# Performance work log

Hardware: AMD Instinct MI355X
Metric: run time of the kernel (lower is better)

## Reference

```python
import jax, jax.numpy as jnp
import numpy as np
import math

D_MODEL = 512
DIM_K = 512
DIM_V = 512
N_HEADS = 8


def setup_inputs() -> dict:
    key = jax.random.key(0)
    ks = jax.random.split(key, 12)
    B, S = 2, 2048
    sc = 1.0 / math.sqrt(D_MODEL)
    return {
        "x": jax.random.normal(ks[0], (B, S, D_MODEL), dtype=jnp.float32),
        "y": jax.random.normal(ks[1], (B, S, D_MODEL), dtype=jnp.float32),
        # weights stored [in, out] so linear is x @ W + b
        "Wq": jax.random.normal(ks[2], (D_MODEL, DIM_K), dtype=jnp.float32) * sc,
        "bq": jnp.zeros((DIM_K,), dtype=jnp.float32),
        "Wk": jax.random.normal(ks[3], (D_MODEL, DIM_K), dtype=jnp.float32) * sc,
        "bk": jnp.zeros((DIM_K,), dtype=jnp.float32),
        "Wv": jax.random.normal(ks[4], (D_MODEL, DIM_V), dtype=jnp.float32) * sc,
        "bv": jnp.zeros((DIM_V,), dtype=jnp.float32),
        "Wo": jax.random.normal(ks[5], (DIM_V, D_MODEL), dtype=jnp.float32) * sc,
        "bo": jnp.zeros((D_MODEL,), dtype=jnp.float32),
    }


def reference(x, y, Wq, bq, Wk, bk, Wv, bv, Wo, bo):
    B, S, _ = x.shape
    H = N_HEADS
    Dh = DIM_K // H
    Dvh = DIM_V // H
    norm = 1.0 / math.sqrt(D_MODEL)  # note: original scales by 1/sqrt(d_model)

    # torch: q(x).reshape(-1, B, S, Dh) -> heads on leading dim (row-major)
    Q = (x @ Wq + bq).reshape(-1, B, S, Dh)      # [H,B,S,Dh]
    K = (y @ Wk + bk).reshape(-1, B, S, Dh)      # [H,B,S,Dh]
    V = (y @ Wv + bv).reshape(-1, B, S, Dvh)     # [H,B,S,Dvh]

    scores = jnp.einsum('hbqd,hbkd->hbqk', Q, K) * norm  # [H,B,S,S]

    # median-threshold mask: torch.median on even n returns lower middle value
    med_idx = (S - 1) // 2
    thre = jnp.sort(scores, axis=-1)[..., med_idx:med_idx + 1]  # [H,B,S,1]
    masked = scores - thre <= 0  # mask where score <= median
    scores = jnp.where(masked, -jnp.inf, scores)

    attn = jax.nn.softmax(scores, axis=-1)
    # dropout omitted (deterministic / eval mode)
    out = jnp.einsum('hbqk,hbkd->hbqd', attn, V)  # [H,B,S,Dvh]
    out = out.reshape(B, S, -1)                   # faithful row-major reshape
    return out @ Wo + bo
```

## Files before the change

kernel.cpp:

```cpp
#include <hip/hip_runtime.h>
#include <hip/hip_bf16.h>
#include <stdint.h>

#define SEQ    2048
#define DMODEL 512
#define NPANEL 16
#define NORM   0.044194173824159216f

typedef _Float16 f16;
typedef __attribute__((ext_vector_type(8))) _Float16 half8;
typedef __attribute__((ext_vector_type(2))) _Float16 half2v;
typedef __attribute__((ext_vector_type(4))) float f32x4;
typedef __attribute__((ext_vector_type(4))) unsigned int u32x4;

__device__ __forceinline__ unsigned umin2(unsigned a, unsigned b){ return a<b?a:b; }
__device__ __forceinline__ unsigned umax2(unsigned a, unsigned b){ return a>b?a:b; }

__global__ __launch_bounds__(256) void k_cvt(const float4* __restrict__ x,
                                             const float4* __restrict__ y,
                                             f16* __restrict__ xh, f16* __restrict__ xl,
                                             f16* __restrict__ yh, f16* __restrict__ yl){
  int i = blockIdx.x*256 + threadIdx.x;
  float4 a = x[i]; float4 b = y[i];
  half2v h0 = {(f16)a.x, (f16)a.y}, h1 = {(f16)a.z, (f16)a.w};
  *(half2v*)(xh + i*4)     = h0; *(half2v*)(xh + i*4 + 2) = h1;
  half2v l0 = {(f16)(a.x-(float)h0[0]), (f16)(a.y-(float)h0[1])};
  half2v l1 = {(f16)(a.z-(float)h1[0]), (f16)(a.w-(float)h1[1])};
  *(half2v*)(xl + i*4)     = l0; *(half2v*)(xl + i*4 + 2) = l1;
  half2v g0 = {(f16)b.x, (f16)b.y}, g1 = {(f16)b.z, (f16)b.w};
  *(half2v*)(yh + i*4)     = g0; *(half2v*)(yh + i*4 + 2) = g1;
  half2v m0 = {(f16)(b.x-(float)g0[0]), (f16)(b.y-(float)g0[1])};
  half2v m1 = {(f16)(b.z-(float)g1[0]), (f16)(b.w-(float)g1[1])};
  *(half2v*)(yl + i*4)     = m0; *(half2v*)(yl + i*4 + 2) = m1;
}

__global__ __launch_bounds__(256) void k_wt(const float* __restrict__ Wq, const float* __restrict__ Wk,
                                            const float* __restrict__ Wv, const float* __restrict__ Wo,
                                            f16* __restrict__ Wth, f16* __restrict__ Wtl){
  int z = blockIdx.z;
  const float* W = (z==0)?Wq:(z==1)?Wk:(z==2)?Wv:Wo;
  __shared__ float tile[64][65];
  int k0 = blockIdx.x*64, n0 = blockIdx.y*64;
  #pragma unroll
  for (int i = 0; i < 16; ++i){
    int s = threadIdx.x + i*256; int kl2 = s>>6, nl = s&63;
    tile[kl2][nl] = W[(k0+kl2)*512 + (n0+nl)];
  }
  __syncthreads();
  #pragma unroll
  for (int i = 0; i < 16; ++i){
    int s = threadIdx.x + i*256; int nl = s>>6, kl2 = s&63;
    float v = tile[kl2][nl];
    f16 h = (f16)v;
    int idx = z*262144 + (n0+nl)*512 + (k0+kl2);
    Wth[idx] = h;
    Wtl[idx] = (f16)(v - (float)h);
  }
}

template<int FINAL>
__global__ __launch_bounds__(256) void k_gemm(const f16* __restrict__ Ah0, const f16* __restrict__ Al0,
                                              const f16* __restrict__ Ah1, const f16* __restrict__ Al1,
                                              const f16* __restrict__ Wh, const f16* __restrict__ Wl,
                                              const float* __restrict__ b0, const float* __restrict__ b1,
                                              const float* __restrict__ b2,
                                              f16* __restrict__ Oq, float* __restrict__ Of){
  int z = blockIdx.z;
  const f16* A  = (z==0) ? Ah0 : Ah1;
  const f16* Alp= (z==0) ? Al0 : Al1;
  const f16* Bh = Wh + z*262144;
  const f16* Bl = Wl + z*262144;
  const float* bias = (z==0)?b0:(z==1)?b1:b2;
  const bool split = (FINAL==0) && (z<2);
  int m0 = blockIdx.x*128, n0 = blockIdx.y*128;

  __shared__ f16 Ahs[128][40], Bhs[128][40], Als[128][40], Bls[128][40];

  int t = threadIdx.x, l = t&63, w = t>>6;
  int wr = w>>1, wc = w&1;
  int lr = l&15, lk = l>>4;

  f32x4 acc[4][4];
  #pragma unroll
  for (int i=0;i<4;++i)
    #pragma unroll
    for (int j=0;j<4;++j) acc[i][j] = (f32x4){0.f,0.f,0.f,0.f};

  for (int ks = 0; ks < 16; ++ks){
    int k0 = ks*32;
    #pragma unroll
    for (int i = 0; i < 2; ++i){
      int s = t + i*256; int r = s>>2, kc = s&3;
      *(u32x4*)(&Ahs[r][kc*8]) = *(const u32x4*)(A   + (m0+r)*512 + k0 + kc*8);
      *(u32x4*)(&Bhs[r][kc*8]) = *(const u32x4*)(Bh  + (n0+r)*512 + k0 + kc*8);
      if (split){
        *(u32x4*)(&Als[r][kc*8]) = *(const u32x4*)(Alp + (m0+r)*512 + k0 + kc*8);
        *(u32x4*)(&Bls[r][kc*8]) = *(const u32x4*)(Bl  + (n0+r)*512 + k0 + kc*8);
      }
    }
    __syncthreads();
    half8 ah[4], bh2[4], al2[4], bl2[4];
    #pragma unroll
    for (int tm = 0; tm < 4; ++tm) ah[tm]  = *(const half8*)(&Ahs[wr*64 + tm*16 + lr][lk*8]);
    #pragma unroll
    for (int tn = 0; tn < 4; ++tn) bh2[tn] = *(const half8*)(&Bhs[wc*64 + tn*16 + lr][lk*8]);
    if (split){
      #pragma unroll
      for (int tm = 0; tm < 4; ++tm) al2[tm] = *(const half8*)(&Als[wr*64 + tm*16 + lr][lk*8]);
      #pragma unroll
      for (int tn = 0; tn < 4; ++tn) bl2[tn] = *(const half8*)(&Bls[wc*64 + tn*16 + lr][lk*8]);
    }
    #pragma unroll
    for (int tm = 0; tm < 4; ++tm)
      #pragma unroll
      for (int tn = 0; tn < 4; ++tn){
        acc[tm][tn] = __builtin_amdgcn_mfma_f32_16x16x32_f16(ah[tm], bh2[tn], acc[tm][tn], 0,0,0);
        if (split){
          acc[tm][tn] = __builtin_amdgcn_mfma_f32_16x16x32_f16(ah[tm], bl2[tn], acc[tm][tn], 0,0,0);
          acc[tm][tn] = __builtin_amdgcn_mfma_f32_16x16x32_f16(al2[tm], bh2[tn], acc[tm][tn], 0,0,0);
        }
      }
    __syncthreads();
  }

  #pragma unroll
  for (int tn = 0; tn < 4; ++tn){
    int n_g = n0 + wc*64 + tn*16 + lr;
    float bv = bias[n_g];
    #pragma unroll
    for (int tm = 0; tm < 4; ++tm){
      #pragma unroll
      for (int r = 0; r < 4; ++r){
        int m_g = m0 + wr*64 + tm*16 + lk*4 + r;
        float v = acc[tm][tn][r] + bv;
        size_t idx = (size_t)m_g*512 + n_g;
        if (FINAL){
          Of[idx] = v;
        } else if (z < 2){
          f16 h = (f16)v;
          Oq[(size_t)z*4194304 + idx] = h;
          Oq[(size_t)z*4194304 + 2097152 + idx] = (f16)(v - (float)h);
        } else {
          Oq[(size_t)4*2097152 + idx] = (f16)v;
        }
      }
    }
  }
}

__global__ __launch_bounds__(256) void k_vt(const unsigned short* __restrict__ V, unsigned short* __restrict__ Vt){
  int p = blockIdx.y;
  int t = threadIdx.x;
  int d = t & 63, sc = t >> 6;
  int s0b = blockIdx.x*32 + sc*8;
  const unsigned short* Vp = V + p*131072;
  unsigned short* Vtp = Vt + p*131072;
  typedef __attribute__((ext_vector_type(8))) short short8;
  short8 vv;
  #pragma unroll
  for (int j = 0; j < 8; ++j) vv[j] = (short)Vp[(s0b + j)*64 + d];
  *(short8*)(Vtp + d*2048 + s0b) = vv;
}

__global__ __launch_bounds__(512, 4) void k_attn(const f16* __restrict__ Qh, const f16* __restrict__ Ql,
                                                 const f16* __restrict__ Kh, const f16* __restrict__ Kl,
                                                 const f16* __restrict__ Vt, f16* __restrict__ O){
  extern __shared__ char scb[];
  __shared__ float rzs[16];
  __shared__ float red[1024];
  int p = blockIdx.y, qt = blockIdx.x;
  int s0 = qt*16;
  const f16* Qhp = Qh + p*131072;
  const f16* Qlp = Ql + p*131072;
  const f16* Khp = Kh + p*131072;
  const f16* Klp = Kl + p*131072;
  const f16* Vtp = Vt + p*131072;
  int t = threadIdx.x, l = t&63, w = t>>6;
  int lr = l&15, lk = l>>4;

  half8 qh[2], ql[2];
  #pragma unroll
  for (int f = 0; f < 2; ++f){
    qh[f] = *(const half8*)(Qhp + (s0+lr)*64 + f*32 + lk*8);
    ql[f] = *(const half8*)(Qlp + (s0+lr)*64 + f*32 + lk*8);
  }

  {
    int cbase = w*128;
    #pragma unroll 2
    for (int ct = 0; ct < 8; ++ct){
      int n = cbase + ct*16;
      const f16* kb  = Khp + (n+lr)*64 + lk*8;
      const f16* kb2 = Klp + (n+lr)*64 + lk*8;
      half8 kh0 = *(const half8*)(kb),  kh1 = *(const half8*)(kb + 32);
      half8 kl0 = *(const half8*)(kb2), kl1 = *(const half8*)(kb2 + 32);
      f32x4 acc = (f32x4){0.f,0.f,0.f,0.f};
      acc = __builtin_amdgcn_mfma_f32_16x16x32_f16(qh[0], kh0, acc, 0,0,0);
      acc = __builtin_amdgcn_mfma_f32_16x16x32_f16(qh[1], kh1, acc, 0,0,0);
      acc = __builtin_amdgcn_mfma_f32_16x16x32_f16(qh[0], kl0, acc, 0,0,0);
      acc = __builtin_amdgcn_mfma_f32_16x16x32_f16(qh[1], kl1, acc, 0,0,0);
      acc = __builtin_amdgcn_mfma_f32_16x16x32_f16(ql[0], kh0, acc, 0,0,0);
      acc = __builtin_amdgcn_mfma_f32_16x16x32_f16(ql[1], kh1, acc, 0,0,0);
      #pragma unroll
      for (int r = 0; r < 4; ++r){
        int row = lk*4 + r;
        *(float*)(scb + row*4096 + (((unsigned)((n + lr)*4)) ^ ((unsigned)(lk<<6)))) = acc[r];
      }
    }
  }
  __syncthreads();

  unsigned ovA0[16], ovA1[16];
  {
    int row0 = w*2;
    unsigned C = ((unsigned)((row0>>2)&3))<<6;
    const char* rb0 = scb + row0*4096;
    const char* rb1 = rb0 + 4096;
    #pragma unroll
    for (int j = 0; j < 16; ++j){
      unsigned off = (((unsigned)((l + j*64)*4)) ^ C);
      unsigned u0 = *(const unsigned*)(rb0 + off);
      unsigned u1 = *(const unsigned*)(rb1 + off);
      ovA0[j] = ((int)u0 < 0) ? ~u0 : (u0 | 0x80000000u);
      ovA1[j] = ((int)u1 < 0) ? ~u1 : (u1 | 0x80000000u);
    }
  }
  __syncthreads();

  {
    int cbase = w*128;
    #pragma unroll 2
    for (int ct = 0; ct < 8; ++ct){
      int n = cbase + ct*16;
      const f16* kb  = Khp + (1024 + n + lr)*64 + lk*8;
      const f16* kb2 = Klp + (1024 + n + lr)*64 + lk*8;
      half8 kh0 = *(const half8*)(kb),  kh1 = *(const half8*)(kb + 32);
      half8 kl0 = *(const half8*)(kb2), kl1 = *(const half8*)(kb2 + 32);
      f32x4 acc = (f32x4){0.f,0.f,0.f,0.f};
      acc = __builtin_amdgcn_mfma_f32_16x16x32_f16(qh[0], kh0, acc, 0,0,0);
      acc = __builtin_amdgcn_mfma_f32_16x16x32_f16(qh[1], kh1, acc, 0,0,0);
      acc = __builtin_amdgcn_mfma_f32_16x16x32_f16(qh[0], kl0, acc, 0,0,0);
      acc = __builtin_amdgcn_mfma_f32_16x16x32_f16(qh[1], kl1, acc, 0,0,0);
      acc = __builtin_amdgcn_mfma_f32_16x16x32_f16(ql[0], kh0, acc, 0,0,0);
      acc = __builtin_amdgcn_mfma_f32_16x16x32_f16(ql[1], kh1, acc, 0,0,0);
      #pragma unroll
      for (int r = 0; r < 4; ++r){
        int row = lk*4 + r;
        *(float*)(scb + row*4096 + (((unsigned)((n + lr)*4)) ^ ((unsigned)(lk<<6)))) = acc[r];
      }
    }
  }
  __syncthreads();

  #pragma unroll
  for (int rr = 0; rr < 2; ++rr){
    int row = w*2 + rr;
    const char* rb = scb + row*4096;
    unsigned C = ((unsigned)((row>>2)&3))<<6;
    unsigned o2[16];
    #pragma unroll
    for (int j = 0; j < 16; ++j){
      unsigned u = *(const unsigned*)(rb + (((unsigned)((l + j*64)*4)) ^ C));
      o2[j] = ((int)u < 0) ? ~u : (u | 0x80000000u);
    }
    unsigned umn = 0xFFFFFFFFu, umx = 0u;
    #pragma unroll
    for (int j = 0; j < 16; ++j){
      unsigned a = (rr==0) ? ovA0[j] : ovA1[j];
      umn = umin2(umn, umin2(a, o2[j]));
      umx = umax2(umax2(umx, a), o2[j]);
    }
    #pragma unroll
    for (int off2 = 1; off2 < 64; off2 <<= 1){
      umn = umin2(umn, (unsigned)__shfl_xor((int)umn, off2));
      umx = umax2(umax2(umx, (unsigned)__shfl_xor((int)umx, off2)), umx);
    }
    unsigned thr;
    {
      unsigned L = umn, R = umx;
      #pragma unroll 1
      for (;;){
        if (L >= R){ thr = R; break; }
        unsigned mid = L + ((R - L) >> 1);
        int c = 0;
        #pragma unroll
        for (int j = 0; j < 16; ++j){
          unsigned a = (rr==0) ? ovA0[j] : ovA1[j];
          c += (int)__popcll(__ballot(a <= mid));
          c += (int)__popcll(__ballot(o2[j] <= mid));
        }
        if (c == 1024){ thr = mid; break; }
        if (c > 1024) R = mid; else L = mid + 1;
      }
    }
    unsigned bmx = (umx & 0x80000000u) ? (umx & 0x7FFFFFFFu) : ~umx;
    float mx = __uint_as_float(bmx);
    float zs = 0.f;
    unsigned g = ((unsigned)(row & 7)) << 4;
    char* pb = scb + row*4096;
    #pragma unroll
    for (int j = 0; j < 32; ++j){
      unsigned a = (j < 16) ? ((rr==0) ? ovA0[j] : ovA1[j]) : o2[j-16];
      unsigned b = (a & 0x80000000u) ? (a & 0x7FFFFFFFu) : ~a;
      float v = __uint_as_float(b);
      float wgt = (a <= thr) ? 0.f : __expf((v - mx) * NORM);
      zs += wgt;
      unsigned col = (unsigned)((j & 15)*64 + l + (j >> 4)*1024);
      *(f16*)(pb + (((col*2)) ^ g)) = (f16)wgt;
    }
    #pragma unroll
    for (int off2 = 1; off2 < 64; off2 <<= 1) zs += __shfl_xor(zs, off2);
    if (l == 0) rzs[row] = 1.f / zs;
  }
  __syncthreads();

  int oc = w & 3, kh2 = w >> 2;
  f32x4 oa = (f32x4){0.f,0.f,0.f,0.f};
  #pragma unroll 4
  for (int kc = 0; kc < 32; ++kc){
    int kbase = kh2*1024 + kc*32;
    half8 pa = *(const half8*)(scb + lr*4096 + (((unsigned)((kbase + lk*8)*2)) ^ (((unsigned)(lr & 7)) << 4)));
    half8 vb = *(const half8*)(Vtp + (oc*16 + lr)*2048 + kbase + lk*8);
    oa = __builtin_amdgcn_mfma_f32_16x16x32_f16(pa, vb, oa, 0,0,0);
  }
  if (kh2 == 1){
    #pragma unroll
    for (int r = 0; r < 4; ++r) red[oc*256 + (lk*4+r)*16 + lr] = oa[r];
  }
  __syncthreads();
  if (kh2 == 0){
    #pragma unroll
    for (int r = 0; r < 4; ++r){
      int row = lk*4 + r;
      float v = (oa[r] + red[oc*256 + row*16 + lr]) * rzs[row];
      O[p*131072 + (s0+row)*64 + oc*16 + lr] = (f16)v;
    }
  }
}

extern "C" void kernel_launch(void* const* d_in, const int* in_sizes, int n_in,
                              void* d_out, int out_size, void* d_ws, size_t ws_size,
                              hipStream_t stream) {
  const float* x  = (const float*)d_in[0];
  const float* y  = (const float*)d_in[1];
  const float* Wq = (const float*)d_in[2];
  const float* bq = (const float*)d_in[3];
  const float* Wk = (const float*)d_in[4];
  const float* bk = (const float*)d_in[5];
  const float* Wv = (const float*)d_in[6];
  const float* bv = (const float*)d_in[7];
  const float* Wo = (const float*)d_in[8];
  const float* bo = (const float*)d_in[9];

  f16* ws = (f16*)d_ws;
  f16* xh  = ws;
  f16* xl  = ws + 2097152;
  f16* yh  = ws + 4194304;
  f16* yl  = ws + 6291456;
  f16* Wth = ws + 8388608;
  f16* Wtl = ws + 9437184;
  f16* QKV = ws + 10485760;
  f16* Vt  = ws;
  f16* Ob  = ws + 2097152;

  (void)hipFuncSetAttribute(reinterpret_cast<const void*>(k_attn),
                            hipFuncAttributeMaxDynamicSharedMemorySize, 65536);

  k_cvt<<<2048, 256, 0, stream>>>((const float4*)x, (const float4*)y, xh, xl, yh, yl);
  k_wt<<<dim3(8,8,4), 256, 0, stream>>>(Wq, Wk, Wv, Wo, Wth, Wtl);
  k_gemm<0><<<dim3(32,4,3), 256, 0, stream>>>(xh, xl, yh, yl, Wth, Wtl, bq, bk, bv, QKV, nullptr);
  k_vt<<<dim3(64,16), 256, 0, stream>>>((const unsigned short*)(QKV + 4*2097152), (unsigned short*)Vt);
  k_attn<<<dim3(128,16), 512, 65536, stream>>>(QKV, QKV + 2097152, QKV + 2*2097152, QKV + 3*2097152, Vt, Ob);
  k_gemm<1><<<dim3(32,4,1), 256, 0, stream>>>(Ob, Ob, Ob, Ob, Wth + 3*262144, Wtl, bo, bo, bo, nullptr, (float*)d_out);
}
```

Baseline: 289.4 us.

## Split fused attention into score, median-select and PV kernels via workspace

```diff
diff --git a/kernel.cpp b/kernel.cpp
--- a/kernel.cpp
+++ b/kernel.cpp
@@ -162,6 +162,127 @@
   *(short8*)(Vtp + d*2048 + s0b) = vv;
 }
 
+__global__ __launch_bounds__(512, 6) void k_score(const f16* __restrict__ Qh, const f16* __restrict__ Ql,
+                                                  const f16* __restrict__ Kh, const f16* __restrict__ Kl,
+                                                  float* __restrict__ S){
+  int p = blockIdx.x, qt = blockIdx.y;
+  int s0 = qt*16;
+  const f16* Qhp = Qh + p*131072;
+  const f16* Qlp = Ql + p*131072;
+  const f16* Khp = Kh + p*131072;
+  const f16* Klp = Kl + p*131072;
+  int t = threadIdx.x, l = t&63, w = t>>6;
+  int lr = l&15, lk = l>>4;
+
+  half8 qh[2], qlo[2];
+  #pragma unroll
+  for (int f = 0; f < 2; ++f){
+    qh[f]  = *(const half8*)(Qhp + (s0+lr)*64 + f*32 + lk*8);
+    qlo[f] = *(const half8*)(Qlp + (s0+lr)*64 + f*32 + lk*8);
+  }
+  float* Sb = S + (size_t)(p*2048 + s0)*2048;
+
+  #pragma unroll 2
+  for (int ct = 0; ct < 16; ++ct){
+    int n = w*256 + ct*16;
+    const f16* kb = Khp + (n+lr)*64 + lk*8;
+    const f16* lb = Klp + (n+lr)*64 + lk*8;
+    half8 kh0 = *(const half8*)(kb);
+    half8 kh1 = *(const half8*)(kb + 32);
+    half8 kl0 = *(const half8*)(lb);
+    half8 kl1 = *(const half8*)(lb + 32);
+    f32x4 c1 = (f32x4){0.f,0.f,0.f,0.f};
+    f32x4 c2 = (f32x4){0.f,0.f,0.f,0.f};
+    f32x4 c3 = (f32x4){0.f,0.f,0.f,0.f};
+    c1 = __builtin_amdgcn_mfma_f32_16x16x32_f16(qh[0],  kh0, c1, 0,0,0);
+    c2 = __builtin_amdgcn_mfma_f32_16x16x32_f16(qh[0],  kl0, c2, 0,0,0);
+    c3 = __builtin_amdgcn_mfma_f32_16x16x32_f16(qlo[0], kh0, c3, 0,0,0);
+    c1 = __builtin_amdgcn_mfma_f32_16x16x32_f16(qh[1],  kh1, c1, 0,0,0);
+    c2 = __builtin_amdgcn_mfma_f32_16x16x32_f16(qh[1],  kl1, c2, 0,0,0);
+    c3 = __builtin_amdgcn_mfma_f32_16x16x32_f16(qlo[1], kh1, c3, 0,0,0);
+    #pragma unroll
+    for (int r = 0; r < 4; ++r){
+      Sb[(size_t)(lk*4 + r)*2048 + n + lr] = c1[r] + c2[r] + c3[r];
+    }
+  }
+}
+
+__global__ __launch_bounds__(256, 6) void k_sel(const float* S, f16* P, float* __restrict__ rz){
+  int wid = blockIdx.x*4 + (threadIdx.x>>6);
+  int l = threadIdx.x & 63;
+  const float* row = S + (size_t)wid*2048;
+  unsigned ov[32];
+  #pragma unroll
+  for (int j = 0; j < 32; ++j){
+    unsigned u = __float_as_uint(row[l + j*64]);
+    ov[j] = ((int)u < 0) ? ~u : (u | 0x80000000u);
+  }
+  unsigned umn = 0xFFFFFFFFu, umx = 0u;
+  #pragma unroll
+  for (int j = 0; j < 32; ++j){ umn = umin2(umn, ov[j]); umx = umax2(umx, ov[j]); }
+  #pragma unroll
+  for (int off2 = 1; off2 < 64; off2 <<= 1){
+    umn = umin2(umn, (unsigned)__shfl_xor((int)umn, off2));
+    umx = umax2(umx, (unsigned)__shfl_xor((int)umx, off2));
+  }
+  unsigned thr;
+  {
+    unsigned L = umn, R = umx;
+    #pragma unroll 1
+    for (;;){
+      if (L >= R){ thr = R; break; }
+      unsigned mid = L + ((R - L) >> 1);
+      int c = 0;
+      #pragma unroll
+      for (int j = 0; j < 32; ++j) c += (int)__popcll(__ballot(ov[j] <= mid));
+      if (c == 1024){ thr = mid; break; }
+      if (c > 1024) R = mid; else L = mid + 1;
+    }
+  }
+  unsigned bmx = (umx & 0x80000000u) ? (umx & 0x7FFFFFFFu) : ~umx;
+  float mx = __uint_as_float(bmx);
+  float zs = 0.f;
+  f16* prow = P + (size_t)wid*4096;
+  #pragma unroll
+  for (int j = 0; j < 32; ++j){
+    unsigned a = ov[j];
+    unsigned b = (a & 0x80000000u) ? (a & 0x7FFFFFFFu) : ~a;
+    float v = __uint_as_float(b);
+    float wgt = (a <= thr) ? 0.f : __expf((v - mx) * NORM);
+    zs += wgt;
+    prow[l + j*64] = (f16)wgt;
+  }
+  #pragma unroll
+  for (int off2 = 1; off2 < 64; off2 <<= 1) zs += __shfl_xor(zs, off2);
+  if (l == 0) rz[wid] = 1.f / zs;
+}
+
+__global__ __launch_bounds__(512, 8) void k_pv(const f16* __restrict__ P, const f16* __restrict__ Vt,
+                                               const float* __restrict__ rz, f16* __restrict__ O){
+  int p = blockIdx.x, rt = blockIdx.y;
+  int t = threadIdx.x, l = t&63, w = t>>6;
+  int lr = l&15, lk = l>>4;
+  int wr = w>>2, oc = w&3;
+  int r0 = rt*32 + wr*16;
+  const f16* prow = P + (size_t)(p*2048 + r0 + lr)*4096 + lk*8;
+  const f16* vb   = Vt + p*131072 + (oc*16 + lr)*2048 + lk*8;
+  f32x4 o0 = (f32x4){0.f,0.f,0.f,0.f};
+  f32x4 o1 = (f32x4){0.f,0.f,0.f,0.f};
+  #pragma unroll 4
+  for (int kc = 0; kc < 64; ++kc){
+    half8 pa = *(const half8*)(prow + kc*32);
+    half8 vv = *(const half8*)(vb + kc*32);
+    if (kc & 1) o1 = __builtin_amdgcn_mfma_f32_16x16x32_f16(pa, vv, o1, 0,0,0);
+    else        o0 = __builtin_amdgcn_mfma_f32_16x16x32_f16(pa, vv, o0, 0,0,0);
+  }
+  #pragma unroll
+  for (int r = 0; r < 4; ++r){
+    int g = r0 + lk*4 + r;
+    float val = (o0[r] + o1[r]) * rz[p*2048 + g];
+    O[p*131072 + g*64 + oc*16 + lr] = (f16)val;
+  }
+}
+
 __global__ __launch_bounds__(512, 4) void k_attn(const f16* __restrict__ Qh, const f16* __restrict__ Ql,
                                                  const f16* __restrict__ Kh, const f16* __restrict__ Kl,
                                                  const f16* __restrict__ Vt, f16* __restrict__ O){
@@ -252,7 +373,7 @@
   }
   __syncthreads();
 
-  #pragma unroll
+  #pragma unroll 1
   for (int rr = 0; rr < 2; ++rr){
     int row = w*2 + rr;
     const char* rb = scb + row*4096;
@@ -273,7 +394,7 @@
     #pragma unroll
     for (int off2 = 1; off2 < 64; off2 <<= 1){
       umn = umin2(umn, (unsigned)__shfl_xor((int)umn, off2));
-      umx = umax2(umax2(umx, (unsigned)__shfl_xor((int)umx, off2)), umx);
+      umx = umax2(umx, (unsigned)__shfl_xor((int)umx, off2));
     }
     unsigned thr;
     {
@@ -306,7 +427,7 @@
       float wgt = (a <= thr) ? 0.f : __expf((v - mx) * NORM);
       zs += wgt;
       unsigned col = (unsigned)((j & 15)*64 + l + (j >> 4)*1024);
-      *(f16*)(pb + (((col*2)) ^ g)) = (f16)wgt;
+      *(f16*)(pb + ((col*2) ^ g)) = (f16)wgt;
     }
     #pragma unroll
     for (int off2 = 1; off2 < 64; off2 <<= 1) zs += __shfl_xor(zs, off2);
@@ -363,13 +484,28 @@
   f16* Vt  = ws;
   f16* Ob  = ws + 2097152;
 
-  (void)hipFuncSetAttribute(reinterpret_cast<const void*>(k_attn),
-                            hipFuncAttributeMaxDynamicSharedMemorySize, 65536);
+  const size_t S_off  = 41943040ULL;
+  const size_t S_size = 268435456ULL;
+  const size_t rz_off = S_off + S_size;
+  const size_t NEED   = rz_off + 131072ULL;
+  bool use_split = (ws_size >= NEED);
 
   k_cvt<<<2048, 256, 0, stream>>>((const float4*)x, (const float4*)y, xh, xl, yh, yl);
   k_wt<<<dim3(8,8,4), 256, 0, stream>>>(Wq, Wk, Wv, Wo, Wth, Wtl);
   k_gemm<0><<<dim3(32,4,3), 256, 0, stream>>>(xh, xl, yh, yl, Wth, Wtl, bq, bk, bv, QKV, nullptr);
   k_vt<<<dim3(64,16), 256, 0, stream>>>((const unsigned short*)(QKV + 4*2097152), (unsigned short*)Vt);
-  k_attn<<<dim3(128,16), 512, 65536, stream>>>(QKV, QKV + 2097152, QKV + 2*2097152, QKV + 3*2097152, Vt, Ob);
+
+  if (use_split){
+    float* S  = (float*)((char*)d_ws + S_off);
+    float* rz = (float*)((char*)d_ws + rz_off);
+    k_score<<<dim3(16,128), 512, 0, stream>>>(QKV, QKV + 2097152, QKV + 2*2097152, QKV + 3*2097152, S);
+    k_sel<<<dim3(8192), 256, 0, stream>>>(S, (f16*)S, rz);
+    k_pv<<<dim3(16,64), 512, 0, stream>>>((const f16*)S, Vt, rz, Ob);
+  } else {
+    (void)hipFuncSetAttribute(reinterpret_cast<const void*>(k_attn),
+                              hipFuncAttributeMaxDynamicSharedMemorySize, 65536);
+    k_attn<<<dim3(128,16), 512, 65536, stream>>>(QKV, QKV + 2097152, QKV + 2*2097152, QKV + 3*2097152, Vt, Ob);
+  }
+
   k_gemm<1><<<dim3(32,4,1), 256, 0, stream>>>(Ob, Ob, Ob, Ob, Wth + 3*262144, Wtl, bo, bo, bo, nullptr, (float*)d_out);
 }
```

Result: no change. 287.7 us (-0.6%).

## Swap attention grid order and split MFMA accumulators into independent chains

Applied to the files above, without the earlier changes.

```diff
diff --git a/kernel.cpp b/kernel.cpp
--- a/kernel.cpp
+++ b/kernel.cpp
@@ -168,7 +168,7 @@
   extern __shared__ char scb[];
   __shared__ float rzs[16];
   __shared__ float red[1024];
-  int p = blockIdx.y, qt = blockIdx.x;
+  int p = blockIdx.x, qt = blockIdx.y;
   int s0 = qt*16;
   const f16* Qhp = Qh + p*131072;
   const f16* Qlp = Ql + p*131072;
@@ -185,74 +185,53 @@
     ql[f] = *(const half8*)(Qlp + (s0+lr)*64 + f*32 + lk*8);
   }
 
-  {
-    int cbase = w*128;
-    #pragma unroll 2
+  unsigned ovA0[16], ovA1[16];
+
+  #pragma unroll 1
+  for (int ph = 0; ph < 2; ++ph){
+    const f16* ka = Khp + ((ph<<10) + w*128 + lr)*64 + lk*8;
+    const f16* la = Klp + ((ph<<10) + w*128 + lr)*64 + lk*8;
+    int n = w*128 + lr;
+    #pragma unroll 1
     for (int ct = 0; ct < 8; ++ct){
-      int n = cbase + ct*16;
-      const f16* kb  = Khp + (n+lr)*64 + lk*8;
-      const f16* kb2 = Klp + (n+lr)*64 + lk*8;
-      half8 kh0 = *(const half8*)(kb),  kh1 = *(const half8*)(kb + 32);
-      half8 kl0 = *(const half8*)(kb2), kl1 = *(const half8*)(kb2 + 32);
-      f32x4 acc = (f32x4){0.f,0.f,0.f,0.f};
-      acc = __builtin_amdgcn_mfma_f32_16x16x32_f16(qh[0], kh0, acc, 0,0,0);
-      acc = __builtin_amdgcn_mfma_f32_16x16x32_f16(qh[1], kh1, acc, 0,0,0);
-      acc = __builtin_amdgcn_mfma_f32_16x16x32_f16(qh[0], kl0, acc, 0,0,0);
-      acc = __builtin_amdgcn_mfma_f32_16x16x32_f16(qh[1], kl1, acc, 0,0,0);
-      acc = __builtin_amdgcn_mfma_f32_16x16x32_f16(ql[0], kh0, acc, 0,0,0);
-      acc = __builtin_amdgcn_mfma_f32_16x16x32_f16(ql[1], kh1, acc, 0,0,0);
+      half8 kb0 = *(const half8*)(ka);
+      half8 kb1 = *(const half8*)(ka + 32);
+      half8 lb0 = *(const half8*)(la);
+      half8 lb1 = *(const half8*)(la + 32);
+      f32x4 c1 = (f32x4){0.f,0.f,0.f,0.f};
+      f32x4 c2 = (f32x4){0.f,0.f,0.f,0.f};
+      f32x4 c3 = (f32x4){0.f,0.f,0.f,0.f};
+      c1 = __builtin_amdgcn_mfma_f32_16x16x32_f16(qh[0], kb0, c1, 0,0,0);
+      c2 = __builtin_amdgcn_mfma_f32_16x16x32_f16(qh[0], lb0, c2, 0,0,0);
+      c3 = __builtin_amdgcn_mfma_f32_16x16x32_f16(ql[0], kb0, c3, 0,0,0);
+      c1 = __builtin_amdgcn_mfma_f32_16x16x32_f16(qh[1], kb1, c1, 0,0,0);
+      c2 = __builtin_amdgcn_mfma_f32_16x16x32_f16(qh[1], lb1, c2, 0,0,0);
+      c3 = __builtin_amdgcn_mfma_f32_16x16x32_f16(ql[1], kb1, c3, 0,0,0);
       #pragma unroll
       for (int r = 0; r < 4; ++r){
         int row = lk*4 + r;
-        *(float*)(scb + row*4096 + (((unsigned)((n + lr)*4)) ^ ((unsigned)(lk<<6)))) = acc[r];
-      }
-    }
-  }
-  __syncthreads();
-
-  unsigned ovA0[16], ovA1[16];
-  {
-    int row0 = w*2;
-    unsigned C = ((unsigned)((row0>>2)&3))<<6;
-    const char* rb0 = scb + row0*4096;
-    const char* rb1 = rb0 + 4096;
-    #pragma unroll
-    for (int j = 0; j < 16; ++j){
-      unsigned off = (((unsigned)((l + j*64)*4)) ^ C);
-      unsigned u0 = *(const unsigned*)(rb0 + off);
-      unsigned u1 = *(const unsigned*)(rb1 + off);
-      ovA0[j] = ((int)u0 < 0) ? ~u0 : (u0 | 0x80000000u);
-      ovA1[j] = ((int)u1 < 0) ? ~u1 : (u1 | 0x80000000u);
-    }
-  }
-  __syncthreads();
-
-  {
-    int cbase = w*128;
-    #pragma unroll 2
-    for (int ct = 0; ct < 8; ++ct){
-      int n = cbase + ct*16;
-      const f16* kb  = Khp + (1024 + n + lr)*64 + lk*8;
-      const f16* kb2 = Klp + (1024 + n + lr)*64 + lk*8;
-      half8 kh0 = *(const half8*)(kb),  kh1 = *(const half8*)(kb + 32);
-      half8 kl0 = *(const half8*)(kb2), kl1 = *(const half8*)(kb2 + 32);
-      f32x4 acc = (f32x4){0.f,0.f,0.f,0.f};
-      acc = __builtin_amdgcn_mfma_f32_16x16x32_f16(qh[0], kh0, acc, 0,0,0);
-      acc = __builtin_amdgcn_mfma_f32_16x16x32_f16(qh[1], kh1, acc, 0,0,0);
-      acc = __builtin_amdgcn_mfma_f32_16x16x32_f16(qh[0], kl0, acc, 0,0,0);
-      acc = __builtin_amdgcn_mfma_f32_16x16x32_f16(qh[1], kl1, acc, 0,0,0);
-      acc = __builtin_amdgcn_mfma_f32_16x16x32_f16(ql[0], kh0, acc, 0,0,0);
-      acc = __builtin_amdgcn_mfma_f32_16x16x32_f16(ql[1], kh1, acc, 0,0,0);
-      #pragma unroll
-      for (int r = 0; r < 4; ++r){
-        int row = lk*4 + r;
-        *(float*)(scb + row*4096 + (((unsigned)((n + lr)*4)) ^ ((unsigned)(lk<<6)))) = acc[r];
-      }
-    }
-  }
-  __syncthreads();
-
-  #pragma unroll
+        *(float*)(scb + row*4096 + (((unsigned)(n*4)) ^ ((unsigned)(lk<<6)))) = c1[r] + c2[r] + c3[r];
+      }
+      ka += 1024; la += 1024; n += 16;
+    }
+    __syncthreads();
+    if (ph == 0){
+      unsigned C = ((unsigned)((w>>1)&3))<<6;
+      const char* rb0 = scb + (w*2)*4096;
+      const char* rb1 = rb0 + 4096;
+      #pragma unroll
+      for (int j = 0; j < 16; ++j){
+        unsigned off = (((unsigned)((l + j*64)*4)) ^ C);
+        unsigned u0 = *(const unsigned*)(rb0 + off);
+        unsigned u1 = *(const unsigned*)(rb1 + off);
+        ovA0[j] = ((int)u0 < 0) ? ~u0 : (u0 | 0x80000000u);
+        ovA1[j] = ((int)u1 < 0) ? ~u1 : (u1 | 0x80000000u);
+      }
+      __syncthreads();
+    }
+  }
+
+  #pragma unroll 1
   for (int rr = 0; rr < 2; ++rr){
     int row = w*2 + rr;
     const char* rb = scb + row*4096;
@@ -273,7 +252,7 @@
     #pragma unroll
     for (int off2 = 1; off2 < 64; off2 <<= 1){
       umn = umin2(umn, (unsigned)__shfl_xor((int)umn, off2));
-      umx = umax2(umax2(umx, (unsigned)__shfl_xor((int)umx, off2)), umx);
+      umx = umax2(umx, (unsigned)__shfl_xor((int)umx, off2));
     }
     unsigned thr;
     {
@@ -306,7 +285,7 @@
       float wgt = (a <= thr) ? 0.f : __expf((v - mx) * NORM);
       zs += wgt;
       unsigned col = (unsigned)((j & 15)*64 + l + (j >> 4)*1024);
-      *(f16*)(pb + (((col*2)) ^ g)) = (f16)wgt;
+      *(f16*)(pb + ((col*2) ^ g)) = (f16)wgt;
     }
     #pragma unroll
     for (int off2 = 1; off2 < 64; off2 <<= 1) zs += __shfl_xor(zs, off2);
@@ -315,14 +294,25 @@
   __syncthreads();
 
   int oc = w & 3, kh2 = w >> 2;
-  f32x4 oa = (f32x4){0.f,0.f,0.f,0.f};
-  #pragma unroll 4
-  for (int kc = 0; kc < 32; ++kc){
-    int kbase = kh2*1024 + kc*32;
-    half8 pa = *(const half8*)(scb + lr*4096 + (((unsigned)((kbase + lk*8)*2)) ^ (((unsigned)(lr & 7)) << 4)));
-    half8 vb = *(const half8*)(Vtp + (oc*16 + lr)*2048 + kbase + lk*8);
-    oa = __builtin_amdgcn_mfma_f32_16x16x32_f16(pa, vb, oa, 0,0,0);
-  }
+  const f16* vb = Vtp + (oc*16 + lr)*2048 + kh2*1024 + lk*8;
+  const char* pbase = scb + lr*4096;
+  unsigned pswz = ((unsigned)(lr & 7)) << 4;
+  unsigned pk = (unsigned)(kh2*1024 + lk*8);
+  f32x4 o0 = (f32x4){0.f,0.f,0.f,0.f};
+  f32x4 o1 = (f32x4){0.f,0.f,0.f,0.f};
+  #pragma unroll 1
+  for (int it = 0; it < 16; ++it){
+    half8 pa0 = *(const half8*)(pbase + (((pk)*2) ^ pswz));
+    half8 vb0 = *(const half8*)(vb);
+    half8 pa1 = *(const half8*)(pbase + (((pk + 32)*2) ^ pswz));
+    half8 vb1 = *(const half8*)(vb + 32);
+    o0 = __builtin_amdgcn_mfma_f32_16x16x32_f16(pa0, vb0, o0, 0,0,0);
+    o1 = __builtin_amdgcn_mfma_f32_16x16x32_f16(pa1, vb1, o1, 0,0,0);
+    pk += 64; vb += 64;
+  }
+  f32x4 oa;
+  #pragma unroll
+  for (int r = 0; r < 4; ++r) oa[r] = o0[r] + o1[r];
   if (kh2 == 1){
     #pragma unroll
     for (int r = 0; r < 4; ++r) red[oc*256 + (lk*4+r)*16 + lr] = oa[r];
@@ -370,6 +360,6 @@
   k_wt<<<dim3(8,8,4), 256, 0, stream>>>(Wq, Wk, Wv, Wo, Wth, Wtl);
   k_gemm<0><<<dim3(32,4,3), 256, 0, stream>>>(xh, xl, yh, yl, Wth, Wtl, bq, bk, bv, QKV, nullptr);
   k_vt<<<dim3(64,16), 256, 0, stream>>>((const unsigned short*)(QKV + 4*2097152), (unsigned short*)Vt);
-  k_attn<<<dim3(128,16), 512, 65536, stream>>>(QKV, QKV + 2097152, QKV + 2*2097152, QKV + 3*2097152, Vt, Ob);
+  k_attn<<<dim3(16,128), 512, 65536, stream>>>(QKV, QKV + 2097152, QKV + 2*2097152, QKV + 3*2097152, Vt, Ob);
   k_gemm<1><<<dim3(32,4,1), 256, 0, stream>>>(Ob, Ob, Ob, Ob, Wth + 3*262144, Wtl, bo, bo, bo, nullptr, (float*)d_out);
 }
```

Result: no change. 287.1 us, median of 2 (-0.8%).
